# Performance work log

Hardware: AMD Instinct MI355X
Metric: run time of the kernel (lower is better)

The kernel has to match this reference:

```python
import jax, jax.numpy as jnp
import numpy as np
from jax import lax

B, P, E, H, V, S = 128, 196, 2048, 512, 10000, 21


def setup_inputs() -> dict:
    key = jax.random.key(0)
    ks = jax.random.split(key, 16)
    r = lambda k, shape, s=0.02: (jax.random.normal(k, shape, jnp.float32) * s)
    return {
        "img_features": jax.random.normal(ks[0], (B, P, E), jnp.float32),
        "captions": jax.random.randint(ks[1], (B, S), 0, V),
        "U_w": r(ks[2], (H, H)), "U_b": jnp.zeros((H,), jnp.float32),
        "W_w": r(ks[3], (E, H)), "W_b": jnp.zeros((H,), jnp.float32),
        "v_w": r(ks[4], (H, 1)), "v_b": jnp.zeros((1,), jnp.float32),
        "init_h_w": r(ks[5], (E, H)), "init_h_b": jnp.zeros((H,), jnp.float32),
        "init_c_w": r(ks[6], (E, H)), "init_c_b": jnp.zeros((H,), jnp.float32),
        "f_beta_w": r(ks[7], (H, E)), "f_beta_b": jnp.zeros((E,), jnp.float32),
        "out_w": r(ks[8], (H, V)), "out_b": jnp.zeros((V,), jnp.float32),
        "emb": r(ks[9], (V, H)),
        "lstm_Wih": r(ks[10], (H + E, 4 * H)), "lstm_Whh": r(ks[11], (H, 4 * H)),
        "lstm_bih": jnp.zeros((4 * H,), jnp.float32), "lstm_bhh": jnp.zeros((4 * H,), jnp.float32),
    }


def reference(img_features, captions, U_w, U_b, W_w, W_b, v_w, v_b,
              init_h_w, init_h_b, init_c_w, init_c_b, f_beta_w, f_beta_b,
              out_w, out_b, emb, lstm_Wih, lstm_Whh, lstm_bih, lstm_bhh):
    batch = img_features.shape[0]
    T = captions.shape[1] - 1  # max_timespan (static)

    # init LSTM state from mean-pooled image features
    avg = img_features.mean(axis=1)                       # [B, E]
    h0 = jnp.tanh(avg @ init_h_w + init_h_b)              # [B, H]
    c0 = jnp.tanh(avg @ init_c_w + init_c_b)              # [B, H]

    # precompute W(img_features) once; it does not depend on h
    W_s = img_features @ W_w + W_b                        # [B, P, H]

    # in training mode the original feeds the embedding of word 0 every step
    emb0 = jnp.broadcast_to(emb[0], (batch, emb.shape[1]))  # [B, H]

    def step(carry, _):
        h, c = carry
        # additive attention
        att = jnp.tanh(W_s + (h @ U_w + U_b)[:, None, :])      # [B, P, H]
        e = (att @ v_w)[..., 0] + v_b[0]                        # [B, P]
        alpha = jax.nn.softmax(e, axis=1)                       # [B, P]
        context = jnp.einsum('bp,bpe->be', alpha, img_features) # [B, E]
        # gated context
        gate = jax.nn.sigmoid(h @ f_beta_w + f_beta_b)          # [B, E]
        x = jnp.concatenate([emb0, gate * context], axis=1)     # [B, H+E]
        # LSTMCell (torch gate order i, f, g, o)
        gates = x @ lstm_Wih + lstm_bih + h @ lstm_Whh + lstm_bhh  # [B, 4H]
        i, f, g, o = jnp.split(gates, 4, axis=1)
        i = jax.nn.sigmoid(i); f = jax.nn.sigmoid(f)
        g = jnp.tanh(g); o = jax.nn.sigmoid(o)
        c_new = f * c + i * g
        h_new = o * jnp.tanh(c_new)
        out = h_new @ out_w + out_b                             # [B, V] (dropout = identity, eval)
        return (h_new, c_new), (out, alpha)

    (_, _), (preds, alphas) = lax.scan(step, (h0, c0), None, length=T)
    preds = jnp.transpose(preds, (1, 0, 2))    # [B, T, V]
    alphas = jnp.transpose(alphas, (1, 0, 2))  # [B, T, P]
    return preds, alphas
```

## Files before the change

### kernel.cpp

```cpp
#include <hip/hip_runtime.h>
#include <stdint.h>


typedef unsigned short u16;
typedef unsigned int u32;
typedef __attribute__((ext_vector_type(8))) short bf16x8;
typedef __attribute__((ext_vector_type(4))) float f32x4;

__device__ __forceinline__ float bf2f(u16 u) { return __uint_as_float(((u32)u) << 16); }
__device__ __forceinline__ u16 f2bf(float f) {
  u32 x = __float_as_uint(f);
  u32 r = x + 0x7fffu + ((x >> 16) & 1u);
  return (u16)(r >> 16);
}
__device__ __forceinline__ float tanh_f(float x) {
  x = fminf(15.f, fmaxf(-15.f, x));
  float e = __expf(2.f * x);
  return 1.f - 2.f * __builtin_amdgcn_rcpf(e + 1.f);
}
__device__ __forceinline__ float sigm_f(float x) {
  x = fminf(30.f, fmaxf(-30.f, x));
  return __builtin_amdgcn_rcpf(1.f + __expf(-x));
}

__global__ __launch_bounds__(256) void k_f32_to_bf16(const float* __restrict__ in,
                                                     u16* __restrict__ out) {
  size_t i = ((size_t)blockIdx.x * 256 + threadIdx.x) * 8;
  float4 v0 = *(const float4*)(in + i);
  float4 v1 = *(const float4*)(in + i + 4);
  union { u16 u[8]; uint4 v; } r;
  r.u[0] = f2bf(v0.x); r.u[1] = f2bf(v0.y); r.u[2] = f2bf(v0.z); r.u[3] = f2bf(v0.w);
  r.u[4] = f2bf(v1.x); r.u[5] = f2bf(v1.y); r.u[6] = f2bf(v1.z); r.u[7] = f2bf(v1.w);
  *(uint4*)(out + i) = r.v;
}

__global__ __launch_bounds__(256) void k_avg(const u16* __restrict__ imgb,
                                             u16* __restrict__ avgb) {
  int b = blockIdx.y;
  int c0 = blockIdx.x * 512 + threadIdx.x * 2;
  const u32* p0 = (const u32*)(imgb + (size_t)b * 196 * 2048 + c0);
  float s0 = 0.f, s1 = 0.f;
  for (int p = 0; p < 196; ++p) {
    u32 v = p0[(size_t)p * 1024];
    s0 += bf2f((u16)(v & 0xffff));
    s1 += bf2f((u16)(v >> 16));
  }
  const float inv = 1.f / 196.f;
  u32 o = ((u32)f2bf(s1 * inv) << 16) | (u32)f2bf(s0 * inv);
  *(u32*)(avgb + (size_t)b * 2048 + c0) = o;
}

template <bool PERM>
__global__ __launch_bounds__(256) void k_transpose_bf16(const float* __restrict__ in,
                                                        int R, int C, int Cpad,
                                                        u16* __restrict__ out, int out_ld) {
  __shared__ float tile[32][33];
  int c0 = blockIdx.x * 32, r0 = blockIdx.y * 32;
  int tx = threadIdx.x, ty = threadIdx.y;
#pragma unroll
  for (int i = 0; i < 32; i += 8) {
    int r = r0 + ty + i, c = c0 + tx;
    tile[ty + i][tx] = (r < R && c < C) ? in[(size_t)r * C + c] : 0.f;
  }
  __syncthreads();
#pragma unroll
  for (int i = 0; i < 32; i += 8) {
    int c = c0 + ty + i, r = r0 + tx;
    if (c < Cpad && r < R) {
      int co = PERM ? ((c & 511) * 4 + (c >> 9)) : c;
      out[(size_t)co * out_ld + r] = f2bf(tile[tx][ty + i]);
    }
  }
}

__global__ __launch_bounds__(256) void k_cbias(const float* __restrict__ emb,
                                               const float* __restrict__ Wih,
                                               const float* __restrict__ bih,
                                               const float* __restrict__ bhh,
                                               float* __restrict__ cb) {
  __shared__ float e0[512];
  int tid = threadIdx.x;
  for (int i = tid; i < 512; i += 256) e0[i] = emb[i];
  __syncthreads();
  int n = blockIdx.x * 256 + tid;
  float s = bih[n] + bhh[n];
  for (int k = 0; k < 512; ++k) s += e0[k] * Wih[(size_t)k * 2048 + n];
  cb[(n & 511) * 4 + (n >> 9)] = s;
}

enum { EPI_TANH_H = 0, EPI_TANH_C };

template <int EPI>
__global__ __launch_bounds__(256) void k_gemm64(
    const u16* __restrict__ A, const u16* __restrict__ BT, int K, int Ntiles,
    const float* __restrict__ bias, float* __restrict__ outF, u16* __restrict__ outB) {
  __shared__ __align__(16) u16 Asm[64 * 72];
  __shared__ __align__(16) u16 Bsm[64 * 72];
  int bid = blockIdx.x;
  int mt = bid / Ntiles, nt = bid % Ntiles;
  long m0 = (long)mt * 64, n0 = (long)nt * 64;
  int tid = threadIdx.x, lane = tid & 63, w = tid >> 6;
  int srow = tid >> 3, schk = tid & 7;
  f32x4 acc[4] = {};
  const u16* Ap0 = A + (m0 + srow) * K + schk * 8;
  const u16* Ap1 = A + (m0 + srow + 32) * K + schk * 8;
  const u16* Bp0 = BT + (n0 + srow) * K + schk * 8;
  const u16* Bp1 = BT + (n0 + srow + 32) * K + schk * 8;
  u16* Aw0 = Asm + srow * 72 + schk * 8;
  u16* Aw1 = Asm + (srow + 32) * 72 + schk * 8;
  u16* Bw0 = Bsm + srow * 72 + schk * 8;
  u16* Bw1 = Bsm + (srow + 32) * 72 + schk * 8;
  const u16* Ar = Asm + (w * 16 + (lane & 15)) * 72 + (lane >> 4) * 8;
  const u16* Br = Bsm + (lane & 15) * 72 + (lane >> 4) * 8;
  for (int k0 = 0; k0 < K; k0 += 64) {
    uint4 a0 = *(const uint4*)(Ap0 + k0);
    uint4 a1 = *(const uint4*)(Ap1 + k0);
    uint4 b0 = *(const uint4*)(Bp0 + k0);
    uint4 b1 = *(const uint4*)(Bp1 + k0);
    __syncthreads();
    *(uint4*)Aw0 = a0;
    *(uint4*)Aw1 = a1;
    *(uint4*)Bw0 = b0;
    *(uint4*)Bw1 = b1;
    __syncthreads();
#pragma unroll
    for (int kk = 0; kk < 2; ++kk) {
      bf16x8 af = *(const bf16x8*)(Ar + kk * 32);
#pragma unroll
      for (int sn = 0; sn < 4; ++sn) {
        bf16x8 bfr = *(const bf16x8*)(Br + sn * 16 * 72 + kk * 32);
        acc[sn] = __builtin_amdgcn_mfma_f32_16x16x32_bf16(af, bfr, acc[sn], 0, 0, 0);
      }
    }
  }
  int cb = lane & 15, rb = (lane >> 4) * 4;
#pragma unroll
  for (int sn = 0; sn < 4; ++sn) {
#pragma unroll
    for (int r = 0; r < 4; ++r) {
      long m = m0 + w * 16 + rb + r;
      long n = n0 + sn * 16 + cb;
      float v = acc[sn][r] + bias[n];
      if (EPI == EPI_TANH_H) outB[m * 512 + n] = f2bf(tanh_f(v));
      else outF[m * 512 + n] = tanh_f(v);
    }
  }
}

enum { EPI128_WS = 0, EPI128_OUT };

template <int EPI>
__global__ __launch_bounds__(256) void k_gemm128(
    const u16* __restrict__ A, const u16* __restrict__ BT, int K, int Ntiles,
    const float* __restrict__ bias, float* __restrict__ outF,
    u16* __restrict__ outB, int ncap) {
  __shared__ __align__(16) u16 Asm[128 * 72];
  __shared__ __align__(16) u16 Bsm[128 * 72];
  int bid = blockIdx.x;
  int mt = bid / Ntiles, nt = bid % Ntiles;
  long m0 = (long)mt * 128, n0 = (long)nt * 128;
  int tid = threadIdx.x, lane = tid & 63, w = tid >> 6;
  int wr = w >> 1, wc = w & 1;
  int srow = tid >> 3, schk = tid & 7;
  f32x4 acc[4][4] = {};
  const u16* Ap = A + (m0 + srow) * K + schk * 8;
  const u16* Bp = BT + (n0 + srow) * K + schk * 8;
  u16* Aw = Asm + srow * 72 + schk * 8;
  u16* Bw = Bsm + srow * 72 + schk * 8;
  const u16* Ar = Asm + (wr * 64 + (lane & 15)) * 72 + (lane >> 4) * 8;
  const u16* Br = Bsm + (wc * 64 + (lane & 15)) * 72 + (lane >> 4) * 8;
  for (int k0 = 0; k0 < K; k0 += 64) {
    uint4 a0 = *(const uint4*)(Ap + k0);
    uint4 a1 = *(const uint4*)(Ap + (size_t)32 * K + k0);
    uint4 a2 = *(const uint4*)(Ap + (size_t)64 * K + k0);
    uint4 a3 = *(const uint4*)(Ap + (size_t)96 * K + k0);
    uint4 b0 = *(const uint4*)(Bp + k0);
    uint4 b1 = *(const uint4*)(Bp + (size_t)32 * K + k0);
    uint4 b2 = *(const uint4*)(Bp + (size_t)64 * K + k0);
    uint4 b3 = *(const uint4*)(Bp + (size_t)96 * K + k0);
    __syncthreads();
    *(uint4*)Aw = a0;
    *(uint4*)(Aw + 32 * 72) = a1;
    *(uint4*)(Aw + 64 * 72) = a2;
    *(uint4*)(Aw + 96 * 72) = a3;
    *(uint4*)Bw = b0;
    *(uint4*)(Bw + 32 * 72) = b1;
    *(uint4*)(Bw + 64 * 72) = b2;
    *(uint4*)(Bw + 96 * 72) = b3;
    __syncthreads();
#pragma unroll
    for (int kk = 0; kk < 2; ++kk) {
      bf16x8 af[4], bfv[4];
#pragma unroll
      for (int i = 0; i < 4; ++i) {
        af[i] = *(const bf16x8*)(Ar + i * 16 * 72 + kk * 32);
        bfv[i] = *(const bf16x8*)(Br + i * 16 * 72 + kk * 32);
      }
#pragma unroll
      for (int sm = 0; sm < 4; ++sm)
#pragma unroll
        for (int sn = 0; sn < 4; ++sn)
          acc[sm][sn] = __builtin_amdgcn_mfma_f32_16x16x32_bf16(af[sm], bfv[sn],
                                                                acc[sm][sn], 0, 0, 0);
    }
  }
  int cb = lane & 15, rb = (lane >> 4) * 4;
#pragma unroll
  for (int sm = 0; sm < 4; ++sm) {
#pragma unroll
    for (int sn = 0; sn < 4; ++sn) {
#pragma unroll
      for (int r = 0; r < 4; ++r) {
        long m = m0 + wr * 64 + sm * 16 + rb + r;
        long n = n0 + wc * 64 + sn * 16 + cb;
        float v = acc[sm][sn][r];
        if (EPI == EPI128_WS) {
          outB[m * 512 + n] = f2bf(v + bias[n]);
        } else {
          if (n < ncap) {
            long t = m >> 7, b = m & 127;
            outF[b * 200000 + t * 10000 + n] = v + bias[n];
          }
        }
      }
    }
  }
}

__global__ __launch_bounds__(256) void k_stepA(
    const u16* __restrict__ hb, const u16* __restrict__ UwB,
    const float* __restrict__ U_b, const float* __restrict__ v_w,
    const u16* __restrict__ WsB, const u16* __restrict__ imgb,
    const u16* __restrict__ fWhT, const float* __restrict__ fb_b,
    float* __restrict__ ctx, float* __restrict__ pre1,
    float* __restrict__ alphas_t) {
  __shared__ __align__(16) char smem[46080];
  int bid = blockIdx.x, tid = threadIdx.x;
  int lane = tid & 63, w = tid >> 6;
  if (bid < 128) {
    int b = bid;
    float* h_s = (float*)smem;
    float* v_s = (float*)(smem + 2048);
    float* p4 = (float*)(smem + 4096);
    float* al_s = (float*)(smem + 12288);
    float* ctxp = (float*)(smem + 13312);
    {
      u32 hv = *(const u32*)(hb + b * 512 + tid * 2);
      h_s[tid * 2] = bf2f((u16)(hv & 0xffff));
      h_s[tid * 2 + 1] = bf2f((u16)(hv >> 16));
      float2 vv = *(const float2*)(v_w + tid * 2);
      v_s[tid * 2] = vv.x;
      v_s[tid * 2 + 1] = vv.y;
    }
    __syncthreads();
    {
      float acc[8] = {};
      const u16* up = UwB + (size_t)(w * 128) * 512 + lane * 8;
#pragma unroll 4
      for (int k = 0; k < 128; ++k) {
        float hk = h_s[w * 128 + k];
        uint4 uv = *(const uint4*)(up + (size_t)k * 512);
        const u16* uu = (const u16*)&uv;
#pragma unroll
        for (int j = 0; j < 8; ++j) acc[j] += hk * bf2f(uu[j]);
      }
      float* dst = p4 + w * 512 + lane * 8;
#pragma unroll
      for (int j = 0; j < 8; ++j) dst[j] = acc[j];
    }
    __syncthreads();
    {
      int n = tid * 2;
#pragma unroll
      for (int j = 0; j < 2; ++j) {
        float s = U_b[n + j] + p4[n + j] + p4[512 + n + j] + p4[1024 + n + j] +
                  p4[1536 + n + j];
        p4[n + j] = s;
      }
    }
    __syncthreads();
    const float* hu_s = p4;
    for (int p = w; p < 196; p += 4) {
      uint4 pk = *(const uint4*)(WsB + ((size_t)b * 196 + p) * 512 + lane * 8);
      const u16* uu = (const u16*)&pk;
      float e = 0.f;
#pragma unroll
      for (int j = 0; j < 8; ++j) {
        int hch = lane * 8 + j;
        e += tanh_f(bf2f(uu[j]) + hu_s[hch]) * v_s[hch];
      }
#pragma unroll
      for (int off = 32; off; off >>= 1) e += __shfl_xor(e, off);
      if (lane == 0) al_s[p] = e;
    }
    __syncthreads();
    if (w == 0) {
      float mx = -1e30f;
      for (int q = lane; q < 196; q += 64) mx = fmaxf(mx, al_s[q]);
#pragma unroll
      for (int off = 32; off; off >>= 1) mx = fmaxf(mx, __shfl_xor(mx, off));
      float ssum = 0.f;
      for (int q = lane; q < 196; q += 64) {
        float ex = __expf(al_s[q] - mx);
        al_s[q] = ex;
        ssum += ex;
      }
#pragma unroll
      for (int off = 32; off; off >>= 1) ssum += __shfl_xor(ssum, off);
      float inv = 1.f / ssum;
      for (int q = lane; q < 196; q += 64) al_s[q] *= inv;
    }
    __syncthreads();
    if (tid < 196) alphas_t[(size_t)b * 3920 + tid] = al_s[tid];
    {
      float a32[32] = {};
      const u16* ib = imgb + (size_t)b * 196 * 2048 + lane * 32;
      for (int p = w; p < 196; p += 4) {
        float ap = al_s[p];
        const uint4* rp = (const uint4*)(ib + (size_t)p * 2048);
#pragma unroll
        for (int q = 0; q < 4; ++q) {
          uint4 v = rp[q];
          const u16* uu = (const u16*)&v;
#pragma unroll
          for (int j = 0; j < 8; ++j) a32[q * 8 + j] += ap * bf2f(uu[j]);
        }
      }
      float* dst = ctxp + w * 2048 + lane * 32;
#pragma unroll
      for (int j = 0; j < 32; ++j) dst[j] = a32[j];
    }
    __syncthreads();
    {
      int c0 = tid * 8;
#pragma unroll
      for (int j = 0; j < 8; ++j) {
        int c = c0 + j;
        ctx[(size_t)b * 2048 + c] =
            ctxp[c] + ctxp[2048 + c] + ctxp[4096 + c] + ctxp[6144 + c];
      }
    }
  } else {
    u16* Asm = (u16*)smem;
    u16* Bsm = (u16*)(smem + 9216);
    int g = bid - 128;
    int mt = g >> 6, nt = g & 63;
    long m0 = (long)mt * 64, n0 = (long)nt * 64;
    int srow = tid >> 3, schk = tid & 7;
    f32x4 acc[4] = {};
    const u16* Ap0 = hb + (m0 + srow) * 512 + schk * 8;
    const u16* Ap1 = hb + (m0 + srow + 32) * 512 + schk * 8;
    const u16* Bp0 = fWhT + (n0 + srow) * 512 + schk * 8;
    const u16* Bp1 = fWhT + (n0 + srow + 32) * 512 + schk * 8;
    u16* Aw0 = Asm + srow * 72 + schk * 8;
    u16* Aw1 = Asm + (srow + 32) * 72 + schk * 8;
    u16* Bw0 = Bsm + srow * 72 + schk * 8;
    u16* Bw1 = Bsm + (srow + 32) * 72 + schk * 8;
    const u16* Ar = Asm + (w * 16 + (lane & 15)) * 72 + (lane >> 4) * 8;
    const u16* Br = Bsm + (lane & 15) * 72 + (lane >> 4) * 8;
#pragma unroll 1
    for (int k0 = 0; k0 < 512; k0 += 64) {
      uint4 a0 = *(const uint4*)(Ap0 + k0);
      uint4 a1 = *(const uint4*)(Ap1 + k0);
      uint4 b0 = *(const uint4*)(Bp0 + k0);
      uint4 b1 = *(const uint4*)(Bp1 + k0);
      __syncthreads();
      *(uint4*)Aw0 = a0;
      *(uint4*)Aw1 = a1;
      *(uint4*)Bw0 = b0;
      *(uint4*)Bw1 = b1;
      __syncthreads();
#pragma unroll
      for (int kk = 0; kk < 2; ++kk) {
        bf16x8 af = *(const bf16x8*)(Ar + kk * 32);
#pragma unroll
        for (int sn = 0; sn < 4; ++sn) {
          bf16x8 bfr = *(const bf16x8*)(Br + sn * 16 * 72 + kk * 32);
          acc[sn] = __builtin_amdgcn_mfma_f32_16x16x32_bf16(af, bfr, acc[sn], 0, 0, 0);
        }
      }
    }
    int cb = lane & 15, rb = (lane >> 4) * 4;
#pragma unroll
    for (int sn = 0; sn < 4; ++sn) {
#pragma unroll
      for (int r = 0; r < 4; ++r) {
        long m = m0 + w * 16 + rb + r;
        long n = n0 + sn * 16 + cb;
        float v = acc[sn][r];
        if (n < 2048) v += fb_b[n];
        pre1[m * 4096 + n] = v;
      }
    }
  }
}

__global__ __launch_bounds__(256) void k_stepB(
    const float* __restrict__ pre1, const float* __restrict__ ctx,
    const u16* __restrict__ Wc2, const float* __restrict__ cbias,
    float* __restrict__ cbuf, u16* __restrict__ hb, u16* __restrict__ hAll,
    int tstep) {
  __shared__ __align__(16) u16 Asm[32 * 72];
  __shared__ __align__(16) u16 Bsm[64 * 72];
  __shared__ float gtile[32][68];
  int bid = blockIdx.x;
  int mt = bid >> 5, nt = bid & 31;
  int m0 = mt * 32, n0 = nt * 64;
  int tid = threadIdx.x, lane = tid & 63, w = tid >> 6;
  int arow = tid >> 3, achk = tid & 7;
  int brow = tid >> 2, bchk = (tid & 3) * 16;
  f32x4 acc0 = {}, acc1 = {};
  const float* pA = pre1 + (size_t)(m0 + arow) * 4096 + achk * 8;
  const float* pC = ctx + (size_t)(m0 + arow) * 2048 + achk * 8;
  const u16* pB = Wc2 + (size_t)(n0 + brow) * 2048 + bchk;
  u16* Aw = Asm + arow * 72 + achk * 8;
  u16* Bw = Bsm + brow * 72 + bchk;
  const u16* Ar = Asm + (lane & 15) * 72 + (lane >> 4) * 8;
  const u16* Br = Bsm + (w * 16 + (lane & 15)) * 72 + (lane >> 4) * 8;
  for (int k0 = 0; k0 < 2048; k0 += 64) {
    float4 g0 = *(const float4*)(pA + k0);
    float4 g1 = *(const float4*)(pA + k0 + 4);
    float4 c0 = *(const float4*)(pC + k0);
    float4 c1 = *(const float4*)(pC + k0 + 4);
    uint4 b0 = *(const uint4*)(pB + k0);
    uint4 b1 = *(const uint4*)(pB + k0 + 8);
    union { u16 u[8]; uint4 v; } av;
    av.u[0] = f2bf(sigm_f(g0.x) * c0.x);
    av.u[1] = f2bf(sigm_f(g0.y) * c0.y);
    av.u[2] = f2bf(sigm_f(g0.z) * c0.z);
    av.u[3] = f2bf(sigm_f(g0.w) * c0.w);
    av.u[4] = f2bf(sigm_f(g1.x) * c1.x);
    av.u[5] = f2bf(sigm_f(g1.y) * c1.y);
    av.u[6] = f2bf(sigm_f(g1.z) * c1.z);
    av.u[7] = f2bf(sigm_f(g1.w) * c1.w);
    __syncthreads();
    *(uint4*)Aw = av.v;
    *(uint4*)Bw = b0;
    *(uint4*)(Bw + 8) = b1;
    __syncthreads();
#pragma unroll
    for (int kk = 0; kk < 2; ++kk) {
      bf16x8 a0 = *(const bf16x8*)(Ar + kk * 32);
      bf16x8 a1 = *(const bf16x8*)(Ar + 16 * 72 + kk * 32);
      bf16x8 bb = *(const bf16x8*)(Br + kk * 32);
      acc0 = __builtin_amdgcn_mfma_f32_16x16x32_bf16(a0, bb, acc0, 0, 0, 0);
      acc1 = __builtin_amdgcn_mfma_f32_16x16x32_bf16(a1, bb, acc1, 0, 0, 0);
    }
  }
  int cbb = lane & 15, rb = (lane >> 4) * 4;
#pragma unroll
  for (int s = 0; s < 2; ++s) {
#pragma unroll
    for (int r = 0; r < 4; ++r) {
      int m = s * 16 + rb + r;
      int nl = w * 16 + cbb;
      float v = (s ? acc1[r] : acc0[r]) +
                pre1[(size_t)(m0 + m) * 4096 + 2048 + n0 + nl] + cbias[n0 + nl];
      gtile[m][nl] = v;
    }
  }
  __syncthreads();
#pragma unroll
  for (int i = 0; i < 2; ++i) {
    int idx = tid * 2 + i;
    int m = idx >> 4, chl = idx & 15;
    float iv = gtile[m][chl * 4 + 0];
    float fv = gtile[m][chl * 4 + 1];
    float gv = gtile[m][chl * 4 + 2];
    float ov = gtile[m][chl * 4 + 3];
    long bg = m0 + m;
    int ch = (n0 >> 2) + chl;
    long ci = bg * 512 + ch;
    float cn = sigm_f(fv) * cbuf[ci] + sigm_f(iv) * tanh_f(gv);
    float h = sigm_f(ov) * tanh_f(cn);
    cbuf[ci] = cn;
    u16 hv = f2bf(h);
    hb[ci] = hv;
    hAll[((size_t)tstep * 128 + bg) * 512 + ch] = hv;
  }
}

extern "C" void kernel_launch(void* const* d_in, const int* in_sizes, int n_in,
                              void* d_out, int out_size, void* d_ws, size_t ws_size,
                              hipStream_t stream) {
  const float* img = (const float*)d_in[0];
  const float* U_w = (const float*)d_in[2];
  const float* U_b = (const float*)d_in[3];
  const float* W_w = (const float*)d_in[4];
  const float* W_b = (const float*)d_in[5];
  const float* v_w = (const float*)d_in[6];
  const float* ih_w = (const float*)d_in[8];
  const float* ih_b = (const float*)d_in[9];
  const float* ic_w = (const float*)d_in[10];
  const float* ic_b = (const float*)d_in[11];
  const float* fb_w = (const float*)d_in[12];
  const float* fb_b = (const float*)d_in[13];
  const float* out_w = (const float*)d_in[14];
  const float* out_b = (const float*)d_in[15];
  const float* emb = (const float*)d_in[16];
  const float* Wih = (const float*)d_in[17];
  const float* Whh = (const float*)d_in[18];
  const float* bih = (const float*)d_in[19];
  const float* bhh = (const float*)d_in[20];
  float* preds = (float*)d_out;
  float* alphas = (float*)d_out + 25600000;

  char* ws = (char*)d_ws;
  size_t off = 0;
  auto alloc = [&](size_t bytes) {
    void* p = ws + off;
    off = (off + bytes + 255) & ~(size_t)255;
    return p;
  };
  u16* imgb = (u16*)alloc((size_t)128 * 196 * 2048 * 2);
  u16* avgb = (u16*)alloc((size_t)128 * 2048 * 2);
  u16* WsB = (u16*)alloc((size_t)128 * 196 * 512 * 2);
  u16* WwT = (u16*)alloc((size_t)512 * 2048 * 2);
  u16* UwB = (u16*)alloc((size_t)512 * 512 * 2);
  u16* ihT = (u16*)alloc((size_t)512 * 2048 * 2);
  u16* icT = (u16*)alloc((size_t)512 * 2048 * 2);
  u16* fWhT = (u16*)alloc((size_t)4096 * 512 * 2);
  u16* Wc2 = (u16*)alloc((size_t)2048 * 2048 * 2);
  u16* owT = (u16*)alloc((size_t)10112 * 512 * 2);
  float* cbias = (float*)alloc(2048 * 4);
  u16* hb = (u16*)alloc((size_t)128 * 512 * 2);
  float* cbuf = (float*)alloc((size_t)128 * 512 * 4);
  float* ctx = (float*)alloc((size_t)128 * 2048 * 4);
  float* pre1 = (float*)alloc((size_t)128 * 4096 * 4);
  u16* hAll = (u16*)alloc((size_t)2560 * 512 * 2);
  if (off > ws_size) return;
  (void)in_sizes; (void)n_in; (void)out_size;

  dim3 tb(32, 8);
  k_f32_to_bf16<<<25088, 256, 0, stream>>>(img, imgb);
  k_f32_to_bf16<<<128, 256, 0, stream>>>(U_w, UwB);
  k_avg<<<dim3(4, 128), 256, 0, stream>>>(imgb, avgb);
  k_transpose_bf16<false><<<dim3(16, 64), tb, 0, stream>>>(W_w, 2048, 512, 512, WwT, 2048);
  k_transpose_bf16<false><<<dim3(16, 64), tb, 0, stream>>>(ih_w, 2048, 512, 512, ihT, 2048);
  k_transpose_bf16<false><<<dim3(16, 64), tb, 0, stream>>>(ic_w, 2048, 512, 512, icT, 2048);
  k_transpose_bf16<false><<<dim3(64, 16), tb, 0, stream>>>(fb_w, 512, 2048, 2048, fWhT, 512);
  k_transpose_bf16<true><<<dim3(64, 16), tb, 0, stream>>>(Whh, 512, 2048, 2048,
                                                          fWhT + (size_t)2048 * 512, 512);
  k_transpose_bf16<true><<<dim3(64, 64), tb, 0, stream>>>(Wih + 512 * 2048, 2048, 2048,
                                                          2048, Wc2, 2048);
  k_transpose_bf16<false><<<dim3(316, 16), tb, 0, stream>>>(out_w, 512, 10000, 10112, owT, 512);
  k_cbias<<<8, 256, 0, stream>>>(emb, Wih, bih, bhh, cbias);
  k_gemm128<EPI128_WS><<<784, 256, 0, stream>>>(imgb, WwT, 2048, 4, W_b, nullptr, WsB, 0);
  k_gemm64<EPI_TANH_H><<<16, 256, 0, stream>>>(avgb, ihT, 2048, 8, ih_b, nullptr, hb);
  k_gemm64<EPI_TANH_C><<<16, 256, 0, stream>>>(avgb, icT, 2048, 8, ic_b, cbuf, nullptr);

  for (int t = 0; t < 20; ++t) {
    k_stepA<<<256, 256, 0, stream>>>(hb, UwB, U_b, v_w, WsB, imgb, fWhT, fb_b, ctx,
                                     pre1, alphas + (size_t)t * 196);
    k_stepB<<<128, 256, 0, stream>>>(pre1, ctx, Wc2, cbias, cbuf, hb, hAll, t);
  }
  k_gemm128<EPI128_OUT><<<20 * 79, 256, 0, stream>>>(hAll, owT, 512, 79, out_b,
                                                     preds, nullptr, 10000);
}
```

Measured before the change: 2.517 ms.

## Fuse per-step kernels into one persistent cooperative kernel with grid syncs

Replaces the 40 per-timestep launches (stepA then stepB, 20 times) with a single cooperative kernel that loops over timesteps and uses grid.sync between phases. It also retiles the LSTM gate GEMM phase from 128 blocks of 32x64 to 256 blocks of 32x32, so all blocks of the persistent grid take part. The aim is to remove kernel launch overhead and the idle gaps between dependent launches. In exchange it relies on all 256 blocks being co-resident and pays for grid-wide barriers. The restrict qualifiers were also dropped.

```diff
diff --git a/kernel.cpp b/kernel.cpp
--- a/kernel.cpp
+++ b/kernel.cpp
@@ -1,5 +1,8 @@
 #include <hip/hip_runtime.h>
+#include <hip/hip_cooperative_groups.h>
 #include <stdint.h>
+
+namespace cg = cooperative_groups;
 
 
 typedef unsigned short u16;
@@ -227,256 +230,248 @@
   }
 }
 
-__global__ __launch_bounds__(256) void k_stepA(
-    const u16* __restrict__ hb, const u16* __restrict__ UwB,
-    const float* __restrict__ U_b, const float* __restrict__ v_w,
-    const u16* __restrict__ WsB, const u16* __restrict__ imgb,
-    const u16* __restrict__ fWhT, const float* __restrict__ fb_b,
-    float* __restrict__ ctx, float* __restrict__ pre1,
-    float* __restrict__ alphas_t) {
+__global__ __launch_bounds__(256) void k_loop(
+    u16* hb, float* cbuf,
+    const u16* UwB, const float* U_b, const float* v_w,
+    const u16* WsB, const u16* imgb,
+    const u16* fWhT, const float* fb_b,
+    float* ctx, float* pre1,
+    const u16* Wc2, const float* cbias,
+    u16* hAll, float* alphas) {
+  cg::grid_group grid = cg::this_grid();
   __shared__ __align__(16) char smem[46080];
   int bid = blockIdx.x, tid = threadIdx.x;
   int lane = tid & 63, w = tid >> 6;
-  if (bid < 128) {
-    int b = bid;
-    float* h_s = (float*)smem;
-    float* v_s = (float*)(smem + 2048);
-    float* p4 = (float*)(smem + 4096);
-    float* al_s = (float*)(smem + 12288);
-    float* ctxp = (float*)(smem + 13312);
+
+  for (int t = 0; t < 20; ++t) {
+    if (bid < 128) {
+      int b = bid;
+      float* h_s = (float*)smem;
+      float* v_s = (float*)(smem + 2048);
+      float* p4 = (float*)(smem + 4096);
+      float* al_s = (float*)(smem + 12288);
+      float* ctxp = (float*)(smem + 13312);
+      {
+        u32 hv = *(const u32*)(hb + b * 512 + tid * 2);
+        h_s[tid * 2] = bf2f((u16)(hv & 0xffff));
+        h_s[tid * 2 + 1] = bf2f((u16)(hv >> 16));
+        float2 vv = *(const float2*)(v_w + tid * 2);
+        v_s[tid * 2] = vv.x;
+        v_s[tid * 2 + 1] = vv.y;
+      }
+      __syncthreads();
+      {
+        float acc[8] = {};
+        const u16* up = UwB + (size_t)(w * 128) * 512 + lane * 8;
+#pragma unroll 4
+        for (int k = 0; k < 128; ++k) {
+          float hk = h_s[w * 128 + k];
+          uint4 uv = *(const uint4*)(up + (size_t)k * 512);
+          const u16* uu = (const u16*)&uv;
+#pragma unroll
+          for (int j = 0; j < 8; ++j) acc[j] += hk * bf2f(uu[j]);
+        }
+        float* dst = p4 + w * 512 + lane * 8;
+#pragma unroll
+        for (int j = 0; j < 8; ++j) dst[j] = acc[j];
+      }
+      __syncthreads();
+      {
+        int n = tid * 2;
+#pragma unroll
+        for (int j = 0; j < 2; ++j) {
+          p4[n + j] = U_b[n + j] + p4[n + j] + p4[512 + n + j] + p4[1024 + n + j] +
+                      p4[1536 + n + j];
+        }
+      }
+      __syncthreads();
+      const float* hu_s = p4;
+      const u16* wsrow = WsB + (size_t)b * 196 * 512 + lane * 8;
+      for (int p = w; p < 196; p += 4) {
+        uint4 pk = *(const uint4*)(wsrow + (size_t)p * 512);
+        const u16* uu = (const u16*)&pk;
+        float e = 0.f;
+#pragma unroll
+        for (int j = 0; j < 8; ++j) {
+          int hch = lane * 8 + j;
+          e += tanh_f(bf2f(uu[j]) + hu_s[hch]) * v_s[hch];
+        }
+#pragma unroll
+        for (int off = 32; off; off >>= 1) e += __shfl_xor(e, off);
+        if (lane == 0) al_s[p] = e;
+      }
+      __syncthreads();
+      if (w == 0) {
+        float mx = -1e30f;
+        for (int q = lane; q < 196; q += 64) mx = fmaxf(mx, al_s[q]);
+#pragma unroll
+        for (int off = 32; off; off >>= 1) mx = fmaxf(mx, __shfl_xor(mx, off));
+        float ssum = 0.f;
+        for (int q = lane; q < 196; q += 64) {
+          float ex = __expf(al_s[q] - mx);
+          al_s[q] = ex;
+          ssum += ex;
+        }
+#pragma unroll
+        for (int off = 32; off; off >>= 1) ssum += __shfl_xor(ssum, off);
+        float inv = 1.f / ssum;
+        for (int q = lane; q < 196; q += 64) al_s[q] *= inv;
+      }
+      __syncthreads();
+      if (tid < 196) alphas[(size_t)b * 3920 + (size_t)t * 196 + tid] = al_s[tid];
+      {
+        float a32[32] = {};
+        const u16* ib = imgb + (size_t)b * 196 * 2048 + lane * 32;
+        for (int p = w; p < 196; p += 4) {
+          float ap = al_s[p];
+          const uint4* rp = (const uint4*)(ib + (size_t)p * 2048);
+#pragma unroll
+          for (int q = 0; q < 4; ++q) {
+            uint4 v = rp[q];
+            const u16* uu = (const u16*)&v;
+#pragma unroll
+            for (int j = 0; j < 8; ++j) a32[q * 8 + j] += ap * bf2f(uu[j]);
+          }
+        }
+        float* dst = ctxp + w * 2048 + lane * 32;
+#pragma unroll
+        for (int j = 0; j < 32; ++j) dst[j] = a32[j];
+      }
+      __syncthreads();
+      {
+        int c0 = tid * 8;
+#pragma unroll
+        for (int j = 0; j < 8; ++j) {
+          int c = c0 + j;
+          ctx[(size_t)b * 2048 + c] =
+              ctxp[c] + ctxp[2048 + c] + ctxp[4096 + c] + ctxp[6144 + c];
+        }
+      }
+    } else {
+      u16* Asm = (u16*)smem;
+      u16* Bsm = (u16*)(smem + 9216);
+      int g = bid - 128;
+      int mt = g >> 6, nt = g & 63;
+      long m0 = (long)mt * 64, n0 = (long)nt * 64;
+      int srow = tid >> 3, schk = tid & 7;
+      f32x4 acc[4] = {};
+      const u16* Ap0 = hb + (m0 + srow) * 512 + schk * 8;
+      const u16* Ap1 = hb + (m0 + srow + 32) * 512 + schk * 8;
+      const u16* Bp0 = fWhT + (n0 + srow) * 512 + schk * 8;
+      const u16* Bp1 = fWhT + (n0 + srow + 32) * 512 + schk * 8;
+      u16* Aw0 = Asm + srow * 72 + schk * 8;
+      u16* Aw1 = Asm + (srow + 32) * 72 + schk * 8;
+      u16* Bw0 = Bsm + srow * 72 + schk * 8;
+      u16* Bw1 = Bsm + (srow + 32) * 72 + schk * 8;
+      const u16* Ar = Asm + (w * 16 + (lane & 15)) * 72 + (lane >> 4) * 8;
+      const u16* Br = Bsm + (lane & 15) * 72 + (lane >> 4) * 8;
+#pragma unroll 1
+      for (int k0 = 0; k0 < 512; k0 += 64) {
+        uint4 a0 = *(const uint4*)(Ap0 + k0);
+        uint4 a1 = *(const uint4*)(Ap1 + k0);
+        uint4 b0 = *(const uint4*)(Bp0 + k0);
+        uint4 b1 = *(const uint4*)(Bp1 + k0);
+        __syncthreads();
+        *(uint4*)Aw0 = a0;
+        *(uint4*)Aw1 = a1;
+        *(uint4*)Bw0 = b0;
+        *(uint4*)Bw1 = b1;
+        __syncthreads();
+#pragma unroll
+        for (int kk = 0; kk < 2; ++kk) {
+          bf16x8 af = *(const bf16x8*)(Ar + kk * 32);
+#pragma unroll
+          for (int sn = 0; sn < 4; ++sn) {
+            bf16x8 bfr = *(const bf16x8*)(Br + sn * 16 * 72 + kk * 32);
+            acc[sn] = __builtin_amdgcn_mfma_f32_16x16x32_bf16(af, bfr, acc[sn], 0, 0, 0);
+          }
+        }
+      }
+      int cb = lane & 15, rb = (lane >> 4) * 4;
+#pragma unroll
+      for (int sn = 0; sn < 4; ++sn) {
+#pragma unroll
+        for (int r = 0; r < 4; ++r) {
+          long m = m0 + w * 16 + rb + r;
+          long n = n0 + sn * 16 + cb;
+          float v = acc[sn][r];
+          if (n < 2048) v += fb_b[n];
+          pre1[m * 4096 + n] = v;
+        }
+      }
+    }
+    grid.sync();
     {
-      u32 hv = *(const u32*)(hb + b * 512 + tid * 2);
-      h_s[tid * 2] = bf2f((u16)(hv & 0xffff));
-      h_s[tid * 2 + 1] = bf2f((u16)(hv >> 16));
-      float2 vv = *(const float2*)(v_w + tid * 2);
-      v_s[tid * 2] = vv.x;
-      v_s[tid * 2 + 1] = vv.y;
-    }
-    __syncthreads();
-    {
-      float acc[8] = {};
-      const u16* up = UwB + (size_t)(w * 128) * 512 + lane * 8;
-#pragma unroll 4
-      for (int k = 0; k < 128; ++k) {
-        float hk = h_s[w * 128 + k];
-        uint4 uv = *(const uint4*)(up + (size_t)k * 512);
-        const u16* uu = (const u16*)&uv;
-#pragma unroll
-        for (int j = 0; j < 8; ++j) acc[j] += hk * bf2f(uu[j]);
-      }
-      float* dst = p4 + w * 512 + lane * 8;
-#pragma unroll
-      for (int j = 0; j < 8; ++j) dst[j] = acc[j];
-    }
-    __syncthreads();
-    {
-      int n = tid * 2;
-#pragma unroll
-      for (int j = 0; j < 2; ++j) {
-        float s = U_b[n + j] + p4[n + j] + p4[512 + n + j] + p4[1024 + n + j] +
-                  p4[1536 + n + j];
-        p4[n + j] = s;
-      }
-    }
-    __syncthreads();
-    const float* hu_s = p4;
-    for (int p = w; p < 196; p += 4) {
-      uint4 pk = *(const uint4*)(WsB + ((size_t)b * 196 + p) * 512 + lane * 8);
-      const u16* uu = (const u16*)&pk;
-      float e = 0.f;
-#pragma unroll
-      for (int j = 0; j < 8; ++j) {
-        int hch = lane * 8 + j;
-        e += tanh_f(bf2f(uu[j]) + hu_s[hch]) * v_s[hch];
-      }
-#pragma unroll
-      for (int off = 32; off; off >>= 1) e += __shfl_xor(e, off);
-      if (lane == 0) al_s[p] = e;
-    }
-    __syncthreads();
-    if (w == 0) {
-      float mx = -1e30f;
-      for (int q = lane; q < 196; q += 64) mx = fmaxf(mx, al_s[q]);
-#pragma unroll
-      for (int off = 32; off; off >>= 1) mx = fmaxf(mx, __shfl_xor(mx, off));
-      float ssum = 0.f;
-      for (int q = lane; q < 196; q += 64) {
-        float ex = __expf(al_s[q] - mx);
-        al_s[q] = ex;
-        ssum += ex;
-      }
-#pragma unroll
-      for (int off = 32; off; off >>= 1) ssum += __shfl_xor(ssum, off);
-      float inv = 1.f / ssum;
-      for (int q = lane; q < 196; q += 64) al_s[q] *= inv;
-    }
-    __syncthreads();
-    if (tid < 196) alphas_t[(size_t)b * 3920 + tid] = al_s[tid];
-    {
-      float a32[32] = {};
-      const u16* ib = imgb + (size_t)b * 196 * 2048 + lane * 32;
-      for (int p = w; p < 196; p += 4) {
-        float ap = al_s[p];
-        const uint4* rp = (const uint4*)(ib + (size_t)p * 2048);
-#pragma unroll
-        for (int q = 0; q < 4; ++q) {
-          uint4 v = rp[q];
-          const u16* uu = (const u16*)&v;
-#pragma unroll
-          for (int j = 0; j < 8; ++j) a32[q * 8 + j] += ap * bf2f(uu[j]);
-        }
-      }
-      float* dst = ctxp + w * 2048 + lane * 32;
-#pragma unroll
-      for (int j = 0; j < 32; ++j) dst[j] = a32[j];
-    }
-    __syncthreads();
-    {
-      int c0 = tid * 8;
-#pragma unroll
-      for (int j = 0; j < 8; ++j) {
-        int c = c0 + j;
-        ctx[(size_t)b * 2048 + c] =
-            ctxp[c] + ctxp[2048 + c] + ctxp[4096 + c] + ctxp[6144 + c];
-      }
-    }
-  } else {
-    u16* Asm = (u16*)smem;
-    u16* Bsm = (u16*)(smem + 9216);
-    int g = bid - 128;
-    int mt = g >> 6, nt = g & 63;
-    long m0 = (long)mt * 64, n0 = (long)nt * 64;
-    int srow = tid >> 3, schk = tid & 7;
-    f32x4 acc[4] = {};
-    const u16* Ap0 = hb + (m0 + srow) * 512 + schk * 8;
-    const u16* Ap1 = hb + (m0 + srow + 32) * 512 + schk * 8;
-    const u16* Bp0 = fWhT + (n0 + srow) * 512 + schk * 8;
-    const u16* Bp1 = fWhT + (n0 + srow + 32) * 512 + schk * 8;
-    u16* Aw0 = Asm + srow * 72 + schk * 8;
-    u16* Aw1 = Asm + (srow + 32) * 72 + schk * 8;
-    u16* Bw0 = Bsm + srow * 72 + schk * 8;
-    u16* Bw1 = Bsm + (srow + 32) * 72 + schk * 8;
-    const u16* Ar = Asm + (w * 16 + (lane & 15)) * 72 + (lane >> 4) * 8;
-    const u16* Br = Bsm + (lane & 15) * 72 + (lane >> 4) * 8;
+      int mt = bid >> 6, nt = bid & 63;
+      int m0 = mt * 32, n0 = nt * 32;
+      u16* Asm2 = (u16*)smem;
+      u16* Bsm2 = (u16*)(smem + 4608);
+      float* gtile = (float*)(smem + 9216);
+      int arow = tid >> 3, achk = tid & 7;
+      int sm = w >> 1, sn = w & 1;
+      f32x4 acc = {};
+      const float* pA = pre1 + (size_t)(m0 + arow) * 4096 + achk * 8;
+      const float* pC = ctx + (size_t)(m0 + arow) * 2048 + achk * 8;
+      const u16* pB = Wc2 + (size_t)(n0 + arow) * 2048 + achk * 8;
+      u16* Aw = Asm2 + arow * 72 + achk * 8;
+      u16* Bw = Bsm2 + arow * 72 + achk * 8;
+      const u16* Ar = Asm2 + (sm * 16 + (lane & 15)) * 72 + (lane >> 4) * 8;
+      const u16* Br = Bsm2 + (sn * 16 + (lane & 15)) * 72 + (lane >> 4) * 8;
 #pragma unroll 1
-    for (int k0 = 0; k0 < 512; k0 += 64) {
-      uint4 a0 = *(const uint4*)(Ap0 + k0);
-      uint4 a1 = *(const uint4*)(Ap1 + k0);
-      uint4 b0 = *(const uint4*)(Bp0 + k0);
-      uint4 b1 = *(const uint4*)(Bp1 + k0);
-      __syncthreads();
-      *(uint4*)Aw0 = a0;
-      *(uint4*)Aw1 = a1;
-      *(uint4*)Bw0 = b0;
-      *(uint4*)Bw1 = b1;
-      __syncthreads();
-#pragma unroll
-      for (int kk = 0; kk < 2; ++kk) {
-        bf16x8 af = *(const bf16x8*)(Ar + kk * 32);
-#pragma unroll
-        for (int sn = 0; sn < 4; ++sn) {
-          bf16x8 bfr = *(const bf16x8*)(Br + sn * 16 * 72 + kk * 32);
-          acc[sn] = __builtin_amdgcn_mfma_f32_16x16x32_bf16(af, bfr, acc[sn], 0, 0, 0);
-        }
-      }
-    }
-    int cb = lane & 15, rb = (lane >> 4) * 4;
-#pragma unroll
-    for (int sn = 0; sn < 4; ++sn) {
+      for (int k0 = 0; k0 < 2048; k0 += 64) {
+        float4 g0 = *(const float4*)(pA + k0);
+        float4 g1 = *(const float4*)(pA + k0 + 4);
+        float4 c0v = *(const float4*)(pC + k0);
+        float4 c1v = *(const float4*)(pC + k0 + 4);
+        uint4 bv = *(const uint4*)(pB + k0);
+        union { u16 u[8]; uint4 v; } av;
+        av.u[0] = f2bf(sigm_f(g0.x) * c0v.x);
+        av.u[1] = f2bf(sigm_f(g0.y) * c0v.y);
+        av.u[2] = f2bf(sigm_f(g0.z) * c0v.z);
+        av.u[3] = f2bf(sigm_f(g0.w) * c0v.w);
+        av.u[4] = f2bf(sigm_f(g1.x) * c1v.x);
+        av.u[5] = f2bf(sigm_f(g1.y) * c1v.y);
+        av.u[6] = f2bf(sigm_f(g1.z) * c1v.z);
+        av.u[7] = f2bf(sigm_f(g1.w) * c1v.w);
+        __syncthreads();
+        *(uint4*)Aw = av.v;
+        *(uint4*)Bw = bv;
+        __syncthreads();
+#pragma unroll
+        for (int kk = 0; kk < 2; ++kk) {
+          bf16x8 a = *(const bf16x8*)(Ar + kk * 32);
+          bf16x8 b = *(const bf16x8*)(Br + kk * 32);
+          acc = __builtin_amdgcn_mfma_f32_16x16x32_bf16(a, b, acc, 0, 0, 0);
+        }
+      }
+      int cb2 = lane & 15, rb2 = (lane >> 4) * 4;
 #pragma unroll
       for (int r = 0; r < 4; ++r) {
-        long m = m0 + w * 16 + rb + r;
-        long n = n0 + sn * 16 + cb;
-        float v = acc[sn][r];
-        if (n < 2048) v += fb_b[n];
-        pre1[m * 4096 + n] = v;
-      }
-    }
-  }
-}
-
-__global__ __launch_bounds__(256) void k_stepB(
-    const float* __restrict__ pre1, const float* __restrict__ ctx,
-    const u16* __restrict__ Wc2, const float* __restrict__ cbias,
-    float* __restrict__ cbuf, u16* __restrict__ hb, u16* __restrict__ hAll,
-    int tstep) {
-  __shared__ __align__(16) u16 Asm[32 * 72];
-  __shared__ __align__(16) u16 Bsm[64 * 72];
-  __shared__ float gtile[32][68];
-  int bid = blockIdx.x;
-  int mt = bid >> 5, nt = bid & 31;
-  int m0 = mt * 32, n0 = nt * 64;
-  int tid = threadIdx.x, lane = tid & 63, w = tid >> 6;
-  int arow = tid >> 3, achk = tid & 7;
-  int brow = tid >> 2, bchk = (tid & 3) * 16;
-  f32x4 acc0 = {}, acc1 = {};
-  const float* pA = pre1 + (size_t)(m0 + arow) * 4096 + achk * 8;
-  const float* pC = ctx + (size_t)(m0 + arow) * 2048 + achk * 8;
-  const u16* pB = Wc2 + (size_t)(n0 + brow) * 2048 + bchk;
-  u16* Aw = Asm + arow * 72 + achk * 8;
-  u16* Bw = Bsm + brow * 72 + bchk;
-  const u16* Ar = Asm + (lane & 15) * 72 + (lane >> 4) * 8;
-  const u16* Br = Bsm + (w * 16 + (lane & 15)) * 72 + (lane >> 4) * 8;
-  for (int k0 = 0; k0 < 2048; k0 += 64) {
-    float4 g0 = *(const float4*)(pA + k0);
-    float4 g1 = *(const float4*)(pA + k0 + 4);
-    float4 c0 = *(const float4*)(pC + k0);
-    float4 c1 = *(const float4*)(pC + k0 + 4);
-    uint4 b0 = *(const uint4*)(pB + k0);
-    uint4 b1 = *(const uint4*)(pB + k0 + 8);
-    union { u16 u[8]; uint4 v; } av;
-    av.u[0] = f2bf(sigm_f(g0.x) * c0.x);
-    av.u[1] = f2bf(sigm_f(g0.y) * c0.y);
-    av.u[2] = f2bf(sigm_f(g0.z) * c0.z);
-    av.u[3] = f2bf(sigm_f(g0.w) * c0.w);
-    av.u[4] = f2bf(sigm_f(g1.x) * c1.x);
-    av.u[5] = f2bf(sigm_f(g1.y) * c1.y);
-    av.u[6] = f2bf(sigm_f(g1.z) * c1.z);
-    av.u[7] = f2bf(sigm_f(g1.w) * c1.w);
-    __syncthreads();
-    *(uint4*)Aw = av.v;
-    *(uint4*)Bw = b0;
-    *(uint4*)(Bw + 8) = b1;
-    __syncthreads();
-#pragma unroll
-    for (int kk = 0; kk < 2; ++kk) {
-      bf16x8 a0 = *(const bf16x8*)(Ar + kk * 32);
-      bf16x8 a1 = *(const bf16x8*)(Ar + 16 * 72 + kk * 32);
-      bf16x8 bb = *(const bf16x8*)(Br + kk * 32);
-      acc0 = __builtin_amdgcn_mfma_f32_16x16x32_bf16(a0, bb, acc0, 0, 0, 0);
-      acc1 = __builtin_amdgcn_mfma_f32_16x16x32_bf16(a1, bb, acc1, 0, 0, 0);
-    }
-  }
-  int cbb = lane & 15, rb = (lane >> 4) * 4;
-#pragma unroll
-  for (int s = 0; s < 2; ++s) {
-#pragma unroll
-    for (int r = 0; r < 4; ++r) {
-      int m = s * 16 + rb + r;
-      int nl = w * 16 + cbb;
-      float v = (s ? acc1[r] : acc0[r]) +
-                pre1[(size_t)(m0 + m) * 4096 + 2048 + n0 + nl] + cbias[n0 + nl];
-      gtile[m][nl] = v;
-    }
-  }
-  __syncthreads();
-#pragma unroll
-  for (int i = 0; i < 2; ++i) {
-    int idx = tid * 2 + i;
-    int m = idx >> 4, chl = idx & 15;
-    float iv = gtile[m][chl * 4 + 0];
-    float fv = gtile[m][chl * 4 + 1];
-    float gv = gtile[m][chl * 4 + 2];
-    float ov = gtile[m][chl * 4 + 3];
-    long bg = m0 + m;
-    int ch = (n0 >> 2) + chl;
-    long ci = bg * 512 + ch;
-    float cn = sigm_f(fv) * cbuf[ci] + sigm_f(iv) * tanh_f(gv);
-    float h = sigm_f(ov) * tanh_f(cn);
-    cbuf[ci] = cn;
-    u16 hv = f2bf(h);
-    hb[ci] = hv;
-    hAll[((size_t)tstep * 128 + bg) * 512 + ch] = hv;
+        int mrow = sm * 16 + rb2 + r;
+        int ncol = sn * 16 + cb2;
+        gtile[mrow * 36 + ncol] =
+            acc[r] + pre1[(size_t)(m0 + mrow) * 4096 + 2048 + n0 + ncol] +
+            cbias[n0 + ncol];
+      }
+      __syncthreads();
+      {
+        int m = tid >> 3, chl = tid & 7;
+        float iv = gtile[m * 36 + chl * 4 + 0];
+        float fv = gtile[m * 36 + chl * 4 + 1];
+        float gv = gtile[m * 36 + chl * 4 + 2];
+        float ov = gtile[m * 36 + chl * 4 + 3];
+        int bg = m0 + m;
+        int ch = (n0 >> 2) + chl;
+        size_t ci = (size_t)bg * 512 + ch;
+        float cn = sigm_f(fv) * cbuf[ci] + sigm_f(iv) * tanh_f(gv);
+        float hh = sigm_f(ov) * tanh_f(cn);
+        cbuf[ci] = cn;
+        u16 hv = f2bf(hh);
+        hb[ci] = hv;
+        hAll[((size_t)t * 128 + bg) * 512 + ch] = hv;
+      }
+    }
+    grid.sync();
   }
 }
 
@@ -549,11 +544,12 @@
   k_gemm64<EPI_TANH_H><<<16, 256, 0, stream>>>(avgb, ihT, 2048, 8, ih_b, nullptr, hb);
   k_gemm64<EPI_TANH_C><<<16, 256, 0, stream>>>(avgb, icT, 2048, 8, ic_b, cbuf, nullptr);
 
-  for (int t = 0; t < 20; ++t) {
-    k_stepA<<<256, 256, 0, stream>>>(hb, UwB, U_b, v_w, WsB, imgb, fWhT, fb_b, ctx,
-                                     pre1, alphas + (size_t)t * 196);
-    k_stepB<<<128, 256, 0, stream>>>(pre1, ctx, Wc2, cbias, cbuf, hb, hAll, t);
-  }
+  {
+    void* args[] = {&hb, &cbuf, &UwB, &U_b, &v_w, &WsB, &imgb, &fWhT, &fb_b,
+                    &ctx, &pre1, &Wc2, &cbias, &hAll, &alphas};
+    hipLaunchCooperativeKernel((const void*)k_loop, dim3(256), dim3(256), args, 0, stream);
+  }
+
   k_gemm128<EPI128_OUT><<<20 * 79, 256, 0, stream>>>(hAll, owT, 512, 79, out_b,
                                                      preds, nullptr, 10000);
 }
```

Measured after the change: 3.732 ms. +48.2%, slower.
